# Optimization experiments

Hardware: AMD Instinct MI355X
Metric: run time of the kernel (lower is better)

## Reference

```python
import jax, jax.numpy as jnp
import numpy as np
import math

H = 1024          # hidden_size
NUM_LAYERS = 2
V = 32000         # target vocabulary
S = 4096          # source length
W = 64            # window_size
WIN = 2 * W + 1   # max window width (static)
H2 = math.ceil(H / 2)
STD_SQ = (W / 2) ** 2
NEG = -1e30


def setup_inputs() -> dict:
    key = jax.random.key(0)
    ks = jax.random.split(key, 16)
    s = 0.02
    return {
        "source_sentence_length": S,
        "encoder_output": jax.random.normal(ks[0], (S, 1, H), jnp.float32),
        "word": jax.random.randint(ks[1], (1, 1), 0, V),
        "h0": jnp.zeros((NUM_LAYERS, 1, H), jnp.float32),
        "c0": jnp.zeros((NUM_LAYERS, 1, H), jnp.float32),
        "embedding": jax.random.normal(ks[2], (V, H), jnp.float32) * s,
        "lstm_w_ih": jax.random.normal(ks[3], (NUM_LAYERS, 4 * H, H), jnp.float32) * s,
        "lstm_w_hh": jax.random.normal(ks[4], (NUM_LAYERS, 4 * H, H), jnp.float32) * s,
        "lstm_b_ih": jax.random.normal(ks[5], (NUM_LAYERS, 4 * H), jnp.float32) * s,
        "lstm_b_hh": jax.random.normal(ks[6], (NUM_LAYERS, 4 * H), jnp.float32) * s,
        "att_fc1_w": jax.random.normal(ks[7], (H2, H), jnp.float32) * s,
        "att_fc1_b": jax.random.normal(ks[8], (H2,), jnp.float32) * s,
        "att_fc2_w": jax.random.normal(ks[9], (1, H2), jnp.float32) * s,
        "att_fc2_b": jax.random.normal(ks[10], (1,), jnp.float32) * s,
        "fc1_w": jax.random.normal(ks[11], (H, 2 * H), jnp.float32) * s,
        "fc1_b": jax.random.normal(ks[12], (H,), jnp.float32) * s,
        "fc2_w": jax.random.normal(ks[13], (V, H), jnp.float32) * s,
        "fc2_b": jax.random.normal(ks[14], (V,), jnp.float32) * s,
    }


def reference(source_sentence_length, encoder_output, word, h0, c0, embedding,
              lstm_w_ih, lstm_w_hh, lstm_b_ih, lstm_b_hh,
              att_fc1_w, att_fc1_b, att_fc2_w, att_fc2_b,
              fc1_w, fc1_b, fc2_w, fc2_b):
    Sf = jnp.float32(source_sentence_length)
    # embedding lookup (seq=1, batch=1) -> (H,)
    x = embedding[word[0, 0]]
    # stacked LSTM, single time step, torch gate order i,f,g,o
    h_list, c_list = [], []
    for l in range(NUM_LAYERS):
        gates = x @ lstm_w_ih[l].T + lstm_b_ih[l] + h0[l, 0] @ lstm_w_hh[l].T + lstm_b_hh[l]
        i, f, g, o = jnp.split(gates, 4)
        c_new = jax.nn.sigmoid(f) * c0[l, 0] + jax.nn.sigmoid(i) * jnp.tanh(g)
        h_new = jax.nn.sigmoid(o) * jnp.tanh(c_new)
        h_list.append(h_new); c_list.append(c_new)
        x = h_new
    h_n = jnp.stack(h_list)[:, None, :]  # (L,1,H)
    c_n = jnp.stack(c_list)[:, None, :]
    h_t = x  # (H,) decoder output at this step
    # ---- dynamic Gaussian-windowed attention ----
    p = Sf * jax.nn.sigmoid(jnp.tanh(h_t @ att_fc1_w.T + att_fc1_b) @ att_fc2_w.T + att_fc2_b)
    p = p.reshape(())
    ws = jnp.round(jnp.clip(p - W, 0, None)).astype(jnp.int32)                      # clamp(min=0)
    we = jnp.round(jnp.clip(p + W, None, source_sentence_length - 1)).astype(jnp.int32)  # clamp(max=S-1)
    idx = ws + jnp.arange(WIN, dtype=jnp.int32)          # fixed-width window
    valid = idx <= we                                    # replicates [ws:we+1] slice
    h_s = encoder_output[jnp.clip(idx, 0, source_sentence_length - 1), 0, :]
    scores = jnp.where(valid, h_s @ h_t, NEG)
    a = jax.nn.softmax(scores)                           # softmax over window
    gauss = jnp.exp((idx.astype(jnp.float32) - p) / (2.0 * STD_SQ))
    a = jnp.where(valid, a * gauss, 0.0)
    ctx = a @ h_s                                        # (H,)
    # ---- output MLP ----
    out = jnp.tanh(jnp.concatenate([ctx, h_t]) @ fc1_w.T + fc1_b)
    y = jax.nn.log_softmax(out @ fc2_w.T + fc2_b)
    return (y.reshape(1, 1, V), out.reshape(1, 1, H), h_n, c_n, a.reshape(1, 1, WIN))
```

## Files before the change

kernel.cpp:

```cpp
#include <hip/hip_runtime.h>

#define HDIM 1024
#define H4   4096
#define VD   32000
#define WINN 129
#define NEGV (-1e30f)

#define X_    0
#define G_    5120
#define ATT1_ 9216
#define CAT_  9728
#define A_    11776
#define SC_   11908
#define IW_   11912
#define PART_ 12000
#define LOG_  12288

#define O_Y   0
#define O_OUT 32000
#define O_HN  33024
#define O_CN  35072
#define O_A   37120

__device__ __forceinline__ float wred(float v){
  #pragma unroll
  for(int off=32; off; off>>=1) v += __shfl_xor(v, off, 64);
  return v;
}
__device__ __forceinline__ float wmax(float v){
  #pragma unroll
  for(int off=32; off; off>>=1) v = fmaxf(v, __shfl_xor(v, off, 64));
  return v;
}
__device__ __forceinline__ float sigf(float x){ return 1.f/(1.f+expf(-x)); }
__device__ __forceinline__ float dot4(float4 a, float4 b){
  return a.x*b.x + a.y*b.y + a.z*b.z + a.w*b.w;
}


__global__ __launch_bounds__(256) void k_lstm_gemv(
    const float* __restrict__ wih, const float* __restrict__ whh,
    const float* __restrict__ bih, const float* __restrict__ bhh,
    const float* __restrict__ xin, const int* __restrict__ word,
    const float* __restrict__ emb, const float* __restrict__ hin,
    float* __restrict__ gout){
  int gid = blockIdx.x*256 + threadIdx.x;
  int r = gid >> 6, lane = gid & 63;
  const float* xp = word ? (emb + ((size_t)word[0]<<10)) : xin;
  const float* wi = wih + ((size_t)r<<10);
  const float* wh = whh + ((size_t)r<<10);
  float acc = 0.f;
  #pragma unroll
  for (int j=0; j<4; j++){
    int o = lane*4 + 256*j;
    acc += dot4(*(const float4*)(wi+o), *(const float4*)(xp+o));
    acc += dot4(*(const float4*)(wh+o), *(const float4*)(hin+o));
  }
  acc = wred(acc);
  if (lane==0) gout[r] = acc + bih[r] + bhh[r];
}

__global__ __launch_bounds__(256) void k_lstm_act(
    const float* __restrict__ g, const float* __restrict__ c0l,
    float* __restrict__ ws, float* __restrict__ hn, float* __restrict__ cn, int last){
  int j = blockIdx.x*256 + threadIdx.x;
  float gi = g[j], gf = g[1024+j], gg = g[2048+j], go = g[3072+j];
  float c  = sigf(gf)*c0l[j] + sigf(gi)*tanhf(gg);
  float h  = sigf(go)*tanhf(c);
  ws[X_ + j] = h;
  if (last) ws[CAT_ + HDIM + j] = h;
  hn[j] = h;
  cn[j] = c;
}

__global__ __launch_bounds__(256) void k_att1(const float* __restrict__ w,
    const float* __restrict__ b, float* __restrict__ ws){
  int gid = blockIdx.x*256 + threadIdx.x;
  int r = gid >> 6, lane = gid & 63;
  const float* wr = w + ((size_t)r<<10);
  float acc = 0.f;
  #pragma unroll
  for (int j=0; j<4; j++){
    int o = lane*4 + 256*j;
    acc += dot4(*(const float4*)(wr+o), *(const float4*)(ws+X_+o));
  }
  acc = wred(acc);
  if (lane==0) ws[ATT1_ + r] = tanhf(acc + b[r]);
}

__global__ __launch_bounds__(256) void k_scores(const float* __restrict__ enc,
    const int* __restrict__ slen, const float* __restrict__ a2w,
    const float* __restrict__ a2b, float* __restrict__ ws){
  int t = threadIdx.x;
  int lane = t & 63;
  float pacc = 0.f;
  #pragma unroll
  for (int j=0; j<2; j++){
    int o = lane*4 + 256*j;
    pacc += dot4(*(const float4*)(a2w+o), *(const float4*)(ws+ATT1_+o));
  }
  pacc = wred(pacc);
  float Sf = (float)slen[0];
  float p  = Sf * sigf(pacc + a2b[0]);
  int wsi = (int)rintf(fmaxf(p - 64.f, 0.f));
  int wei = (int)rintf(fminf(p + 64.f, Sf - 1.f));
  if (blockIdx.x==0 && t==0){
    ws[SC_] = p;
    ((int*)ws)[IW_]   = wsi;
    ((int*)ws)[IW_+1] = wei;
  }
  int k = blockIdx.x*4 + (t>>6);
  if (k >= WINN) return;
  int idx = wsi + k;
  int smax = slen[0]-1;
  int ci = idx > smax ? smax : (idx < 0 ? 0 : idx);
  const float* er = enc + ((size_t)ci<<10);
  float acc = 0.f;
  #pragma unroll
  for (int j=0; j<4; j++){
    int o = lane*4 + 256*j;
    acc += dot4(*(const float4*)(er+o), *(const float4*)(ws+X_+o));
  }
  acc = wred(acc);
  if (lane==0) ws[A_ + k] = (idx <= wei) ? acc : NEGV;
}

__global__ __launch_bounds__(1024) void k_smctx(const float* __restrict__ enc,
    const int* __restrict__ slen, float* __restrict__ ws, float* __restrict__ aout){
  __shared__ float sarr[WINN];
  __shared__ float av[WINN];
  __shared__ int   ci[WINN];
  __shared__ float red[2];
  int t = threadIdx.x;
  float p = ws[SC_];
  int wsi = ((int*)ws)[IW_], wei = ((int*)ws)[IW_+1];
  int smax = slen[0]-1;
  if (t < WINN){
    sarr[t] = ws[A_ + t];
    int idx = wsi + t;
    ci[t] = idx > smax ? smax : (idx < 0 ? 0 : idx);
  }
  __syncthreads();
  if (t < 64){
    float m = fmaxf(sarr[t], sarr[t+64]);
    if (t==0) m = fmaxf(m, sarr[128]);
    m = wmax(m);
    if (t==0) red[0] = m;
  }
  __syncthreads();
  float M = red[0];
  if (t < 64){
    float e = expf(sarr[t]-M) + expf(sarr[t+64]-M);
    if (t==0) e += expf(sarr[128]-M);
    e = wred(e);
    if (t==0) red[1] = e;
  }
  __syncthreads();
  float sm = red[1];
  if (t < WINN){
    int idx = wsi + t;
    float a = expf(sarr[t]-M) / sm;
    a = (idx <= wei) ? a * expf(((float)idx - p) * (1.f/2048.f)) : 0.f;
    av[t] = a;
    aout[t] = a;
  }
  __syncthreads();
  float acc = 0.f;
  for (int k=0; k<WINN; k++) acc += av[k] * enc[((size_t)ci[k]<<10) + t];
  ws[CAT_ + t] = acc;
}

__global__ __launch_bounds__(256) void k_fc1(const float* __restrict__ w,
    const float* __restrict__ b, float* __restrict__ ws, float* __restrict__ oout){
  int gid = blockIdx.x*256 + threadIdx.x;
  int r = gid >> 6, lane = gid & 63;
  const float* wr = w + ((size_t)r<<11);
  float acc = 0.f;
  #pragma unroll
  for (int j=0; j<8; j++){
    int o = lane*4 + 256*j;
    acc += dot4(*(const float4*)(wr+o), *(const float4*)(ws+CAT_+o));
  }
  acc = wred(acc);
  if (lane==0){
    float o = tanhf(acc + b[r]);
    ws[X_ + r] = o;
    oout[r] = o;
  }
}

__global__ __launch_bounds__(512) void k_fc2(const float* __restrict__ w,
    const float* __restrict__ b, float* __restrict__ ws){
  int gid = blockIdx.x*512 + threadIdx.x;
  int r = gid >> 6, lane = gid & 63;
  const float* wr = w + ((size_t)r<<10);
  float acc = 0.f;
  #pragma unroll
  for (int j=0; j<4; j++){
    int o = lane*4 + 256*j;
    acc += dot4(*(const float4*)(wr+o), *(const float4*)(ws+X_+o));
  }
  acc = wred(acc);
  if (lane==0) ws[LOG_ + r] = acc + b[r];
}

__global__ __launch_bounds__(256) void k_lsepart(float* __restrict__ ws){
  __shared__ float red[4];
  int b = blockIdx.x, t = threadIdx.x;
  int base = b*1024;
  int n = (b==31) ? 256 : 1024;
  bool act = (t*4 < n);
  float4 v = make_float4(0.f,0.f,0.f,0.f);
  if (act) v = *(const float4*)(ws + LOG_ + base + t*4);
  float m = act ? fmaxf(fmaxf(v.x,v.y), fmaxf(v.z,v.w)) : -INFINITY;
  m = wmax(m);
  if ((t&63)==0) red[t>>6] = m;
  __syncthreads();
  float M = fmaxf(fmaxf(red[0],red[1]), fmaxf(red[2],red[3]));
  __syncthreads();
  float s = act ? (expf(v.x-M)+expf(v.y-M)+expf(v.z-M)+expf(v.w-M)) : 0.f;
  s = wred(s);
  if ((t&63)==0) red[t>>6] = s;
  __syncthreads();
  if (t==0){
    ws[PART_ + b]      = M;
    ws[PART_ + 32 + b] = red[0]+red[1]+red[2]+red[3];
  }
}

__global__ __launch_bounds__(256) void k_y(const float* __restrict__ ws, float* __restrict__ y){
  int i = blockIdx.x*256 + threadIdx.x;
  float M = -INFINITY;
  #pragma unroll
  for (int k=0; k<32; k++) M = fmaxf(M, ws[PART_+k]);
  float S = 0.f;
  #pragma unroll
  for (int k=0; k<32; k++) S += ws[PART_+32+k] * expf(ws[PART_+k] - M);
  float off = M + logf(S);
  if (i < 8000){
    float4 v = *(const float4*)(ws + LOG_ + i*4);
    v.x -= off; v.y -= off; v.z -= off; v.w -= off;
    *(float4*)(y + i*4) = v;
  }
}

extern "C" void kernel_launch(void* const* d_in, const int* in_sizes, int n_in,
                              void* d_out, int out_size, void* d_ws, size_t ws_size,
                              hipStream_t stream) {
  const int*   slen = (const int*)d_in[0];
  const float* enc  = (const float*)d_in[1];
  const int*   word = (const int*)d_in[2];
  const float* h0   = (const float*)d_in[3];
  const float* c0   = (const float*)d_in[4];
  const float* emb  = (const float*)d_in[5];
  const float* wih  = (const float*)d_in[6];
  const float* whh  = (const float*)d_in[7];
  const float* bih  = (const float*)d_in[8];
  const float* bhh  = (const float*)d_in[9];
  const float* a1w  = (const float*)d_in[10];
  const float* a1b  = (const float*)d_in[11];
  const float* a2w  = (const float*)d_in[12];
  const float* a2b  = (const float*)d_in[13];
  const float* f1w  = (const float*)d_in[14];
  const float* f1b  = (const float*)d_in[15];
  const float* f2w  = (const float*)d_in[16];
  const float* f2b  = (const float*)d_in[17];
  float* ws  = (float*)d_ws;
  float* out = (float*)d_out;

  k_lstm_gemv<<<1024,256,0,stream>>>(wih, whh, bih, bhh,
                                     nullptr, word, emb, h0, ws + G_);
  k_lstm_act<<<4,256,0,stream>>>(ws + G_, c0, ws, out + O_HN, out + O_CN, 0);
  k_lstm_gemv<<<1024,256,0,stream>>>(wih + (size_t)H4*HDIM, whh + (size_t)H4*HDIM,
                                     bih + H4, bhh + H4,
                                     ws + X_, nullptr, nullptr, h0 + HDIM, ws + G_);
  k_lstm_act<<<4,256,0,stream>>>(ws + G_, c0 + HDIM, ws, out + O_HN + HDIM, out + O_CN + HDIM, 1);

  k_att1<<<128,256,0,stream>>>(a1w, a1b, ws);
  k_scores<<<33,256,0,stream>>>(enc, slen, a2w, a2b, ws);
  k_smctx<<<1,1024,0,stream>>>(enc, slen, ws, out + O_A);
  k_fc1<<<256,256,0,stream>>>(f1w, f1b, ws, out + O_OUT);
  k_fc2<<<4000,512,0,stream>>>(f2w, f2b, ws);
  k_lsepart<<<32,256,0,stream>>>(ws);
  k_y<<<32,256,0,stream>>>(ws, out + O_Y);
}
```

Before: 358.0 us.

## Fuse LSTM gate GEMVs with activations, merge attention kernels, fold LSE partials into fc2

Each LSTM layer now has one kernel in which every wave computes all four gate rows for a hidden unit and applies the activations itself. Layer 1's recurrent GEMV (h0 @ W_hh) is hoisted into the layer-0 kernel because it does not depend on layer 0's output. The window-score and softmax/context kernels are merged into one single-block kernel, and fc2 now computes four rows per wave and emits per-block max/sum partials, which removes the separate LSE partial kernel. The intent is to cut kernel launches and intermediate round trips. In exchange, the window scores are computed by a single block instead of 33, and the final reduction now covers 1000 partials instead of 32.

```diff
diff --git a/kernel.cpp b/kernel.cpp
--- a/kernel.cpp
+++ b/kernel.cpp
@@ -1,20 +1,18 @@
 #include <hip/hip_runtime.h>
 
 #define HDIM 1024
-#define H4   4096
 #define VD   32000
 #define WINN 129
 #define NEGV (-1e30f)
 
-#define X_    0
-#define G_    5120
-#define ATT1_ 9216
-#define CAT_  9728
-#define A_    11776
-#define SC_   11908
-#define IW_   11912
-#define PART_ 12000
-#define LOG_  12288
+#define X_     0
+#define HT_    1024
+#define G_     5120
+#define ATT1_  9216
+#define CAT_   9728
+#define PARTM_ 12000
+#define PARTS_ 13000
+#define LOG_   16384
 
 #define O_Y   0
 #define O_OUT 32000
@@ -36,41 +34,79 @@
 __device__ __forceinline__ float dot4(float4 a, float4 b){
   return a.x*b.x + a.y*b.y + a.z*b.z + a.w*b.w;
 }
-
-
-__global__ __launch_bounds__(256) void k_lstm_gemv(
+__device__ __forceinline__ float4 ld4(const float* p){ return *(const float4*)p; }
+
+
+__global__ __launch_bounds__(256) void k_lstm0(
     const float* __restrict__ wih, const float* __restrict__ whh,
     const float* __restrict__ bih, const float* __restrict__ bhh,
-    const float* __restrict__ xin, const int* __restrict__ word,
-    const float* __restrict__ emb, const float* __restrict__ hin,
-    float* __restrict__ gout){
-  int gid = blockIdx.x*256 + threadIdx.x;
-  int r = gid >> 6, lane = gid & 63;
-  const float* xp = word ? (emb + ((size_t)word[0]<<10)) : xin;
-  const float* wi = wih + ((size_t)r<<10);
-  const float* wh = whh + ((size_t)r<<10);
-  float acc = 0.f;
-  #pragma unroll
-  for (int j=0; j<4; j++){
-    int o = lane*4 + 256*j;
-    acc += dot4(*(const float4*)(wi+o), *(const float4*)(xp+o));
-    acc += dot4(*(const float4*)(wh+o), *(const float4*)(hin+o));
-  }
-  acc = wred(acc);
-  if (lane==0) gout[r] = acc + bih[r] + bhh[r];
-}
-
-__global__ __launch_bounds__(256) void k_lstm_act(
-    const float* __restrict__ g, const float* __restrict__ c0l,
-    float* __restrict__ ws, float* __restrict__ hn, float* __restrict__ cn, int last){
-  int j = blockIdx.x*256 + threadIdx.x;
-  float gi = g[j], gf = g[1024+j], gg = g[2048+j], go = g[3072+j];
-  float c  = sigf(gf)*c0l[j] + sigf(gi)*tanhf(gg);
-  float h  = sigf(go)*tanhf(c);
-  ws[X_ + j] = h;
-  if (last) ws[CAT_ + HDIM + j] = h;
-  hn[j] = h;
-  cn[j] = c;
+    const int* __restrict__ word, const float* __restrict__ emb,
+    const float* __restrict__ h0, const float* __restrict__ c0,
+    float* __restrict__ ws, float* __restrict__ hn, float* __restrict__ cn){
+  int j = blockIdx.x*4 + (threadIdx.x>>6);
+  int lane = threadIdx.x & 63;
+  const float* x    = emb + ((size_t)word[0]<<10);
+  const float* h00  = h0;
+  const float* h01  = h0 + HDIM;
+  const float* wih0 = wih + ((size_t)j<<10);
+  const float* whh0 = whh + ((size_t)j<<10);
+  const float* whh1 = whh + ((size_t)(4096 + j)<<10);
+  float acc[12];
+  #pragma unroll
+  for (int g=0; g<12; g++) acc[g]=0.f;
+  #pragma unroll
+  for (int c=0;c<4;c++){
+    int o = lane*4 + 256*c;
+    float4 xv = ld4(x+o), av = ld4(h00+o), bv = ld4(h01+o);
+    #pragma unroll
+    for (int g=0; g<4; g++){
+      acc[g]   += dot4(ld4(wih0 + ((size_t)g<<20) + o), xv);
+      acc[4+g] += dot4(ld4(whh0 + ((size_t)g<<20) + o), av);
+      acc[8+g] += dot4(ld4(whh1 + ((size_t)g<<20) + o), bv);
+    }
+  }
+  #pragma unroll
+  for (int g=0; g<12; g++) acc[g] = wred(acc[g]);
+  if (lane==0){
+    float gi = acc[0]+acc[4] + bih[j]      + bhh[j];
+    float gf = acc[1]+acc[5] + bih[1024+j] + bhh[1024+j];
+    float gg = acc[2]+acc[6] + bih[2048+j] + bhh[2048+j];
+    float go = acc[3]+acc[7] + bih[3072+j] + bhh[3072+j];
+    float cc = sigf(gf)*c0[j] + sigf(gi)*tanhf(gg);
+    float hh = sigf(go)*tanhf(cc);
+    ws[X_+j] = hh; hn[j]=hh; cn[j]=cc;
+    #pragma unroll
+    for (int g=0; g<4; g++)
+      ws[G_ + g*1024 + j] = acc[8+g] + bih[4096 + g*1024 + j] + bhh[4096 + g*1024 + j];
+  }
+}
+
+__global__ __launch_bounds__(256) void k_lstm1(
+    const float* __restrict__ wih1, const float* __restrict__ c0l,
+    float* __restrict__ ws, float* __restrict__ hn, float* __restrict__ cn){
+  int j = blockIdx.x*4 + (threadIdx.x>>6);
+  int lane = threadIdx.x & 63;
+  const float* wr = wih1 + ((size_t)j<<10);
+  float acc[4] = {0.f,0.f,0.f,0.f};
+  #pragma unroll
+  for (int c=0;c<4;c++){
+    int o = lane*4 + 256*c;
+    float4 hv = ld4(ws + X_ + o);
+    #pragma unroll
+    for (int g=0; g<4; g++)
+      acc[g] += dot4(ld4(wr + ((size_t)g<<20) + o), hv);
+  }
+  #pragma unroll
+  for (int g=0; g<4; g++) acc[g]=wred(acc[g]);
+  if (lane==0){
+    float gi = acc[0] + ws[G_ + j];
+    float gf = acc[1] + ws[G_ + 1024 + j];
+    float gg = acc[2] + ws[G_ + 2048 + j];
+    float go = acc[3] + ws[G_ + 3072 + j];
+    float cc = sigf(gf)*c0l[j] + sigf(gi)*tanhf(gg);
+    float hh = sigf(go)*tanhf(cc);
+    ws[HT_+j]=hh; ws[CAT_+HDIM+j]=hh; hn[j]=hh; cn[j]=cc;
+  }
 }
 
 __global__ __launch_bounds__(256) void k_att1(const float* __restrict__ w,
@@ -82,70 +118,64 @@
   #pragma unroll
   for (int j=0; j<4; j++){
     int o = lane*4 + 256*j;
-    acc += dot4(*(const float4*)(wr+o), *(const float4*)(ws+X_+o));
+    acc += dot4(ld4(wr+o), ld4(ws+HT_+o));
   }
   acc = wred(acc);
   if (lane==0) ws[ATT1_ + r] = tanhf(acc + b[r]);
 }
 
-__global__ __launch_bounds__(256) void k_scores(const float* __restrict__ enc,
+__global__ __launch_bounds__(1024) void k_attn(const float* __restrict__ enc,
     const int* __restrict__ slen, const float* __restrict__ a2w,
-    const float* __restrict__ a2b, float* __restrict__ ws){
-  int t = threadIdx.x;
-  int lane = t & 63;
-  float pacc = 0.f;
-  #pragma unroll
-  for (int j=0; j<2; j++){
-    int o = lane*4 + 256*j;
-    pacc += dot4(*(const float4*)(a2w+o), *(const float4*)(ws+ATT1_+o));
-  }
-  pacc = wred(pacc);
-  float Sf = (float)slen[0];
-  float p  = Sf * sigf(pacc + a2b[0]);
-  int wsi = (int)rintf(fmaxf(p - 64.f, 0.f));
-  int wei = (int)rintf(fminf(p + 64.f, Sf - 1.f));
-  if (blockIdx.x==0 && t==0){
-    ws[SC_] = p;
-    ((int*)ws)[IW_]   = wsi;
-    ((int*)ws)[IW_+1] = wei;
-  }
-  int k = blockIdx.x*4 + (t>>6);
-  if (k >= WINN) return;
-  int idx = wsi + k;
-  int smax = slen[0]-1;
-  int ci = idx > smax ? smax : (idx < 0 ? 0 : idx);
-  const float* er = enc + ((size_t)ci<<10);
-  float acc = 0.f;
-  #pragma unroll
-  for (int j=0; j<4; j++){
-    int o = lane*4 + 256*j;
-    acc += dot4(*(const float4*)(er+o), *(const float4*)(ws+X_+o));
-  }
-  acc = wred(acc);
-  if (lane==0) ws[A_ + k] = (idx <= wei) ? acc : NEGV;
-}
-
-__global__ __launch_bounds__(1024) void k_smctx(const float* __restrict__ enc,
-    const int* __restrict__ slen, float* __restrict__ ws, float* __restrict__ aout){
+    const float* __restrict__ a2b, float* __restrict__ ws, float* __restrict__ aout){
   __shared__ float sarr[WINN];
   __shared__ float av[WINN];
   __shared__ int   ci[WINN];
   __shared__ float red[2];
-  int t = threadIdx.x;
-  float p = ws[SC_];
-  int wsi = ((int*)ws)[IW_], wei = ((int*)ws)[IW_+1];
+  __shared__ float pinfo[1];
+  __shared__ int   iw[2];
+  int t = threadIdx.x, lane = t & 63, wv = t >> 6;
+  float Sf = (float)slen[0];
   int smax = slen[0]-1;
-  if (t < WINN){
-    sarr[t] = ws[A_ + t];
-    int idx = wsi + t;
-    ci[t] = idx > smax ? smax : (idx < 0 ? 0 : idx);
+  if (wv==0){
+    float pacc = 0.f;
+    #pragma unroll
+    for (int c=0;c<2;c++){
+      int o = lane*4 + 256*c;
+      pacc += dot4(ld4(a2w+o), ld4(ws+ATT1_+o));
+    }
+    pacc = wred(pacc);
+    float p = Sf * sigf(pacc + a2b[0]);
+    if (t==0){
+      pinfo[0] = p;
+      iw[0] = (int)rintf(fmaxf(p-64.f,0.f));
+      iw[1] = (int)rintf(fminf(p+64.f, Sf-1.f));
+    }
+  }
+  __syncthreads();
+  float p = pinfo[0];
+  int wsi = iw[0], wei = iw[1];
+  for (int k = wv; k < WINN; k += 16){
+    int idx = wsi + k;
+    int c = idx > smax ? smax : idx;
+    const float* er = enc + ((size_t)c<<10);
+    float acc=0.f;
+    #pragma unroll
+    for (int cc=0;cc<4;cc++){
+      int o = lane*4 + 256*cc;
+      acc += dot4(ld4(er+o), ld4(ws+HT_+o));
+    }
+    acc = wred(acc);
+    if (lane==0){
+      sarr[k] = (idx<=wei)? acc : NEGV;
+      ci[k] = c;
+    }
   }
   __syncthreads();
   if (t < 64){
     float m = fmaxf(sarr[t], sarr[t+64]);
     if (t==0) m = fmaxf(m, sarr[128]);
     m = wmax(m);
-    if (t==0) red[0] = m;
+    if (t==0) red[0]=m;
   }
   __syncthreads();
   float M = red[0];
@@ -153,21 +183,20 @@
     float e = expf(sarr[t]-M) + expf(sarr[t+64]-M);
     if (t==0) e += expf(sarr[128]-M);
     e = wred(e);
-    if (t==0) red[1] = e;
+    if (t==0) red[1]=e;
   }
   __syncthreads();
   float sm = red[1];
   if (t < WINN){
     int idx = wsi + t;
-    float a = expf(sarr[t]-M) / sm;
-    a = (idx <= wei) ? a * expf(((float)idx - p) * (1.f/2048.f)) : 0.f;
-    av[t] = a;
-    aout[t] = a;
-  }
-  __syncthreads();
-  float acc = 0.f;
-  for (int k=0; k<WINN; k++) acc += av[k] * enc[((size_t)ci[k]<<10) + t];
-  ws[CAT_ + t] = acc;
+    float a = expf(sarr[t]-M)/sm;
+    a = (idx<=wei) ? a*expf(((float)idx - p)*(1.f/2048.f)) : 0.f;
+    av[t]=a; aout[t]=a;
+  }
+  __syncthreads();
+  float acc=0.f;
+  for (int k=0;k<WINN;k++) acc += av[k]*enc[((size_t)ci[k]<<10)+t];
+  ws[CAT_+t]=acc;
 }
 
 __global__ __launch_bounds__(256) void k_fc1(const float* __restrict__ w,
@@ -179,7 +208,7 @@
   #pragma unroll
   for (int j=0; j<8; j++){
     int o = lane*4 + 256*j;
-    acc += dot4(*(const float4*)(wr+o), *(const float4*)(ws+CAT_+o));
+    acc += dot4(ld4(wr+o), ld4(ws+CAT_+o));
   }
   acc = wred(acc);
   if (lane==0){
@@ -191,55 +220,63 @@
 
 __global__ __launch_bounds__(512) void k_fc2(const float* __restrict__ w,
     const float* __restrict__ b, float* __restrict__ ws){
-  int gid = blockIdx.x*512 + threadIdx.x;
-  int r = gid >> 6, lane = gid & 63;
-  const float* wr = w + ((size_t)r<<10);
-  float acc = 0.f;
-  #pragma unroll
-  for (int j=0; j<4; j++){
-    int o = lane*4 + 256*j;
-    acc += dot4(*(const float4*)(wr+o), *(const float4*)(ws+X_+o));
-  }
-  acc = wred(acc);
-  if (lane==0) ws[LOG_ + r] = acc + b[r];
-}
-
-__global__ __launch_bounds__(256) void k_lsepart(float* __restrict__ ws){
-  __shared__ float red[4];
-  int b = blockIdx.x, t = threadIdx.x;
-  int base = b*1024;
-  int n = (b==31) ? 256 : 1024;
-  bool act = (t*4 < n);
-  float4 v = make_float4(0.f,0.f,0.f,0.f);
-  if (act) v = *(const float4*)(ws + LOG_ + base + t*4);
-  float m = act ? fmaxf(fmaxf(v.x,v.y), fmaxf(v.z,v.w)) : -INFINITY;
+  __shared__ float lg[32];
+  int wv = threadIdx.x >> 6, lane = threadIdx.x & 63;
+  int r0 = (blockIdx.x*8 + wv)*4;
+  const float* wr = w + ((size_t)r0<<10);
+  float acc[4]={0.f,0.f,0.f,0.f};
+  #pragma unroll
+  for (int c=0;c<4;c++){
+    int o = lane*4 + 256*c;
+    float4 xv = ld4(ws+X_+o);
+    #pragma unroll
+    for (int rr=0;rr<4;rr++)
+      acc[rr] += dot4(ld4(wr + ((size_t)rr<<10) + o), xv);
+  }
+  #pragma unroll
+  for (int rr=0;rr<4;rr++) acc[rr]=wred(acc[rr]);
+  if (lane==0){
+    #pragma unroll
+    for (int rr=0;rr<4;rr++){
+      float v = acc[rr] + b[r0+rr];
+      ws[LOG_+r0+rr] = v;
+      lg[wv*4+rr] = v;
+    }
+  }
+  __syncthreads();
+  int t = threadIdx.x;
+  if (t < 64){
+    float v = (t<32)? lg[t] : -INFINITY;
+    float m = wmax(v);
+    float e = (t<32)? expf(lg[t]-m) : 0.f;
+    float s = wred(e);
+    if (t==0){
+      ws[PARTM_ + blockIdx.x] = m;
+      ws[PARTS_ + blockIdx.x] = s;
+    }
+  }
+}
+
+__global__ __launch_bounds__(256) void k_y(const float* __restrict__ ws, float* __restrict__ y){
+  __shared__ float rm[4], rs[4];
+  int t = threadIdx.x, lane = t&63, wv = t>>6;
+  float m = -INFINITY;
+  for (int k=t;k<1000;k+=256) m = fmaxf(m, ws[PARTM_+k]);
   m = wmax(m);
-  if ((t&63)==0) red[t>>6] = m;
-  __syncthreads();
-  float M = fmaxf(fmaxf(red[0],red[1]), fmaxf(red[2],red[3]));
-  __syncthreads();
-  float s = act ? (expf(v.x-M)+expf(v.y-M)+expf(v.z-M)+expf(v.w-M)) : 0.f;
+  if (lane==0) rm[wv]=m;
+  __syncthreads();
+  float M = fmaxf(fmaxf(rm[0],rm[1]), fmaxf(rm[2],rm[3]));
+  float s = 0.f;
+  for (int k=t;k<1000;k+=256) s += ws[PARTS_+k]*expf(ws[PARTM_+k]-M);
   s = wred(s);
-  if ((t&63)==0) red[t>>6] = s;
-  __syncthreads();
-  if (t==0){
-    ws[PART_ + b]      = M;
-    ws[PART_ + 32 + b] = red[0]+red[1]+red[2]+red[3];
-  }
-}
-
-__global__ __launch_bounds__(256) void k_y(const float* __restrict__ ws, float* __restrict__ y){
-  int i = blockIdx.x*256 + threadIdx.x;
-  float M = -INFINITY;
-  #pragma unroll
-  for (int k=0; k<32; k++) M = fmaxf(M, ws[PART_+k]);
-  float S = 0.f;
-  #pragma unroll
-  for (int k=0; k<32; k++) S += ws[PART_+32+k] * expf(ws[PART_+k] - M);
+  if (lane==0) rs[wv]=s;
+  __syncthreads();
+  float S = rs[0]+rs[1]+rs[2]+rs[3];
   float off = M + logf(S);
+  int i = blockIdx.x*256 + t;
   if (i < 8000){
-    float4 v = *(const float4*)(ws + LOG_ + i*4);
-    v.x -= off; v.y -= off; v.z -= off; v.w -= off;
+    float4 v = ld4(ws + LOG_ + i*4);
+    v.x-=off; v.y-=off; v.z-=off; v.w-=off;
     *(float4*)(y + i*4) = v;
   }
 }
@@ -268,19 +305,13 @@
   float* ws  = (float*)d_ws;
   float* out = (float*)d_out;
 
-  k_lstm_gemv<<<1024,256,0,stream>>>(wih, whh, bih, bhh,
-                                     nullptr, word, emb, h0, ws + G_);
-  k_lstm_act<<<4,256,0,stream>>>(ws + G_, c0, ws, out + O_HN, out + O_CN, 0);
-  k_lstm_gemv<<<1024,256,0,stream>>>(wih + (size_t)H4*HDIM, whh + (size_t)H4*HDIM,
-                                     bih + H4, bhh + H4,
-                                     ws + X_, nullptr, nullptr, h0 + HDIM, ws + G_);
-  k_lstm_act<<<4,256,0,stream>>>(ws + G_, c0 + HDIM, ws, out + O_HN + HDIM, out + O_CN + HDIM, 1);
-
+  k_lstm0<<<256,256,0,stream>>>(wih, whh, bih, bhh, word, emb, h0, c0,
+                                ws, out + O_HN, out + O_CN);
+  k_lstm1<<<256,256,0,stream>>>(wih + (size_t)4096*1024, c0 + HDIM,
+                                ws, out + O_HN + HDIM, out + O_CN + HDIM);
   k_att1<<<128,256,0,stream>>>(a1w, a1b, ws);
-  k_scores<<<33,256,0,stream>>>(enc, slen, a2w, a2b, ws);
-  k_smctx<<<1,1024,0,stream>>>(enc, slen, ws, out + O_A);
+  k_attn<<<1,1024,0,stream>>>(enc, slen, a2w, a2b, ws, out + O_A);
   k_fc1<<<256,256,0,stream>>>(f1w, f1b, ws, out + O_OUT);
-  k_fc2<<<4000,512,0,stream>>>(f2w, f2b, ws);
-  k_lsepart<<<32,256,0,stream>>>(ws);
+  k_fc2<<<1000,512,0,stream>>>(f2w, f2b, ws);
   k_y<<<32,256,0,stream>>>(ws, out + O_Y);
 }
```

New measurement: 361.4 us. Within noise of the previous version (+1.0%).
